# Optimization experiments

Measured on AMD Instinct MI355X. Metric: run time of the kernel, lower is better.

The kernel has to match this reference:

```python
import jax, jax.numpy as jnp
import numpy as np

D_MODEL = 768
N_HEADS = 12
D_K = D_MODEL // N_HEADS
NEG_INF = -1e9


def setup_inputs() -> dict:
    key = jax.random.key(0)
    ks = jax.random.split(key, 7)
    B, S = 4, 2048
    x = jax.random.normal(ks[0], (B, S, D_MODEL), dtype=jnp.float32)
    # causal mask, broadcastable to [B, H, S, S]
    mask = jnp.tril(jnp.ones((S, S), dtype=bool))[None, None, :, :]
    scale = 1.0 / np.sqrt(D_MODEL)
    Wq = jax.random.normal(ks[1], (D_MODEL, D_MODEL), dtype=jnp.float32) * scale
    bq = jnp.zeros((D_MODEL,), dtype=jnp.float32)
    Wk = jax.random.normal(ks[2], (D_MODEL, D_MODEL), dtype=jnp.float32) * scale
    bk = jnp.zeros((D_MODEL,), dtype=jnp.float32)
    Wv = jax.random.normal(ks[3], (D_MODEL, D_MODEL), dtype=jnp.float32) * scale
    bv = jnp.zeros((D_MODEL,), dtype=jnp.float32)
    return {"x": x, "mask": mask, "Wq": Wq, "bq": bq, "Wk": Wk, "bk": bk, "Wv": Wv, "bv": bv}


def reference(x, mask, Wq, bq, Wk, bk, Wv, bv):
    B, S, _ = x.shape
    # projections (torch Linear: y = x @ W.T + b)
    q = (x @ Wq.T + bq).reshape(B, S, N_HEADS, D_K)
    k = (x @ Wk.T + bk).reshape(B, S, N_HEADS, D_K)
    v = (x @ Wv.T + bv).reshape(B, S, N_HEADS, D_K)
    # scores: [B, H, S, S]
    scores = jnp.einsum("bqhd,bkhd->bhqk", q, k) / jnp.sqrt(jnp.float32(D_K))
    scores = jnp.where(mask, scores, NEG_INF)
    probs = jax.nn.softmax(scores, axis=-1)
    # attention: [B, H, S, D_K] -> [B, S, d_model]
    attn = jnp.einsum("bhqk,bkhd->bqhd", probs, v).reshape(B, S, D_MODEL)
    return attn
```

## Files before the change

### kernel.cpp

```cpp
#include <hip/hip_runtime.h>
#include <math.h>


#define S_LEN 2048
#define BATCH 4
#define HEADS 12
#define DM 768
#define DK 64
#define BH (BATCH*HEADS)
#define MROWS (BATCH*S_LEN)
#define QSCALE 0.1803368801111244f

typedef __attribute__((ext_vector_type(8))) short short8;
typedef __attribute__((ext_vector_type(4))) float floatx4;
typedef __attribute__((ext_vector_type(16))) float floatx16;
typedef __attribute__((ext_vector_type(4))) unsigned int uintx4;
typedef __attribute__((address_space(3))) unsigned char lds_byte;
typedef __attribute__((address_space(1))) const unsigned char glob_byte;

__device__ __forceinline__ unsigned short f2bf(float f) {
  union { float f; unsigned int u; } a; a.f = f;
  unsigned int u = a.u;
  return (unsigned short)((u + 0x7fffu + ((u >> 16) & 1u)) >> 16);
}

__global__ __launch_bounds__(256) void cast_all(
    const float* __restrict__ x,
    const float* __restrict__ w0, const float* __restrict__ w1,
    const float* __restrict__ w2,
    unsigned short* __restrict__ xb, unsigned short* __restrict__ wb) {
  const int NX = MROWS * DM, NW = DM * DM;
  int i = (blockIdx.x * 256 + threadIdx.x) * 4;
  const float* src; unsigned short* dst; int off;
  if (i < NX) { src = x; dst = xb; off = i; }
  else {
    int kk = i - NX; int s = kk / NW; off = kk - s * NW;
    src = (s == 0) ? w0 : (s == 1) ? w1 : w2;
    dst = wb + (size_t)s * NW;
  }
  float4 v = *(const float4*)(src + off);
  ushort4 o;
  o.x = f2bf(v.x); o.y = f2bf(v.y); o.z = f2bf(v.z); o.w = f2bf(v.w);
  *(ushort4*)(dst + off) = o;
}

__global__ __launch_bounds__(256) void qkv_gemm(
    const unsigned short* __restrict__ xb,
    const unsigned short* __restrict__ wb,
    const float* __restrict__ bq, const float* __restrict__ bk,
    const float* __restrict__ bv,
    unsigned short* __restrict__ qo,
    unsigned short* __restrict__ ko,
    unsigned short* __restrict__ vto) {
  __shared__ unsigned short a_lds[2 * 128 * 32];
  __shared__ unsigned short b_lds[2 * 128 * 32];
  const int mat = blockIdx.z;
  const int tid = threadIdx.x;
  const int wave = tid >> 6, lane = tid & 63, quad = lane >> 4, ln = lane & 15;
  const int wm = wave & 1, wn = wave >> 1;
  const int m_blk = blockIdx.x * 128, n_blk = blockIdx.y * 128;
  const unsigned short* w = wb + (size_t)mat * DM * DM;
  const int srow_i[2] = { (0 * 256 + wave * 64 + lane) >> 2,
                          (1 * 256 + wave * 64 + lane) >> 2 };
  const int sq = (lane & 3) * 8;

  const floatx4 fz = {0.f, 0.f, 0.f, 0.f};
  floatx4 acc[4][4];
#pragma unroll
  for (int mg = 0; mg < 4; mg++)
#pragma unroll
    for (int c = 0; c < 4; c++) acc[mg][c] = fz;

  for (int k0 = 0; k0 < DM; k0 += 64) {
#pragma unroll
    for (int p = 0; p < 2; p++)
#pragma unroll
      for (int i = 0; i < 2; i++) {
        const int cbase = i * 256 + wave * 64;
        const int row = srow_i[i];
        __builtin_amdgcn_global_load_lds(
            (glob_byte*)(xb + (size_t)(m_blk + row) * DM + k0 + p * 32 + sq),
            (lds_byte*)(a_lds + p * 4096 + cbase * 8), 16, 0, 0);
        __builtin_amdgcn_global_load_lds(
            (glob_byte*)(w + (size_t)(n_blk + row) * DM + k0 + p * 32 + sq),
            (lds_byte*)(b_lds + p * 4096 + cbase * 8), 16, 0, 0);
      }
    __syncthreads();

    short8 af[4][2], bf[4][2];
#pragma unroll
    for (int mg = 0; mg < 4; mg++)
#pragma unroll
      for (int p = 0; p < 2; p++)
        af[mg][p] = *(const short8*)(a_lds + p * 4096 + (wm * 64 + mg * 16 + ln) * 32 + quad * 8);
#pragma unroll
    for (int c = 0; c < 4; c++)
#pragma unroll
      for (int p = 0; p < 2; p++)
        bf[c][p] = *(const short8*)(b_lds + p * 4096 + (wn * 64 + c * 16 + ln) * 32 + quad * 8);
#pragma unroll
    for (int mg = 0; mg < 4; mg++)
#pragma unroll
      for (int c = 0; c < 4; c++) {
        acc[mg][c] = __builtin_amdgcn_mfma_f32_16x16x32_bf16(af[mg][0], bf[c][0], acc[mg][c], 0, 0, 0);
        acc[mg][c] = __builtin_amdgcn_mfma_f32_16x16x32_bf16(af[mg][1], bf[c][1], acc[mg][c], 0, 0, 0);
      }
    __syncthreads();
  }

  const float* bias = (mat == 0) ? bq : (mat == 1) ? bk : bv;
  const float oscale = (mat == 0) ? QSCALE : 1.0f;
  const int m_base = m_blk + wm * 64, n_base = n_blk + wn * 64;
#pragma unroll
  for (int mg = 0; mg < 4; mg++)
#pragma unroll
    for (int c = 0; c < 4; c++) {
      int gn = n_base + c * 16 + ln;
      int hd = gn >> 6, d = gn & 63;
      float bias_v = bias[gn] * oscale;
      int gm0 = m_base + mg * 16 + quad * 4;
      int bb = gm0 >> 11, s0 = gm0 & (S_LEN - 1);
      if (mat == 2) {
        ushort4 pk;
        pk.x = f2bf(acc[mg][c][0] + bias_v);
        pk.y = f2bf(acc[mg][c][1] + bias_v);
        pk.z = f2bf(acc[mg][c][2] + bias_v);
        pk.w = f2bf(acc[mg][c][3] + bias_v);
        *(ushort4*)(vto + (((size_t)(bb * HEADS + hd)) * DK + d) * S_LEN + s0) = pk;
      } else {
        unsigned short* dst = (mat == 0 ? qo : ko) +
            (((size_t)(bb * HEADS + hd)) * S_LEN + s0) * DK + d;
#pragma unroll
        for (int r = 0; r < 4; r++)
          dst[(size_t)r * DK] = f2bf(acc[mg][c][r] * oscale + bias_v);
      }
    }
}

__global__ __launch_bounds__(256) void flash_attn(
    const unsigned short* __restrict__ q,
    const unsigned short* __restrict__ k,
    const unsigned short* __restrict__ vt,
    float* __restrict__ out) {
  __shared__ unsigned short k_lds[2][64 * 64];
  __shared__ unsigned short v_lds[2][64 * 64];
  const int id0 = blockIdx.x;
  const int rr = id0 >> 8, jj = id0 & 255;
  const int g = (rr == 0) ? jj : (rr == 1) ? (511 - jj) : (512 + jj);
  const int bh = g % BH;
  const int qt = (S_LEN / 128 - 1) - (g / BH);
  const int q0 = qt * 128;
  const int tid = threadIdx.x;
  const int wave = tid >> 6, lane = tid & 63;
  const int l31 = lane & 31, hi = lane >> 5;
  const unsigned short* qp = q + (size_t)bh * S_LEN * DK;
  const unsigned char* kpb = (const unsigned char*)(k  + (size_t)bh * S_LEN * DK);
  const unsigned char* vpb = (const unsigned char*)(vt + (size_t)bh * DK * S_LEN);
  const int qr_base = q0 + wave * 32;

  const floatx16 fz16 = {0.f,0.f,0.f,0.f,0.f,0.f,0.f,0.f,
                         0.f,0.f,0.f,0.f,0.f,0.f,0.f,0.f};

  short8 ones;
#pragma unroll
  for (int j = 0; j < 8; j++) ones[j] = (short)0x3F80;

  short8 aq[4];
#pragma unroll
  for (int ks = 0; ks < 4; ks++)
    aq[ks] = *(const short8*)(qp + (size_t)(qr_base + l31) * DK + ks * 16 + hi * 8);

  floatx16 o0 = fz16, o1 = fz16, lacc = fz16;

  const int sc0 = tid, sc1 = 256 + tid;
  const int sr[2]  = { sc0 >> 3, sc1 >> 3 };
  const int ssb[2] = { ((sc0 & 7) * 16) ^ ((sr[0] & 7) << 4),
                       ((sc1 & 7) * 16) ^ ((sr[1] & 7) << 4) };

  auto stage = [&](int nb, int k0) {
    unsigned short* kd = &k_lds[nb][0];
    unsigned short* vd = &v_lds[nb][0];
#pragma unroll
    for (int i = 0; i < 2; i++) {
      const int cbase = i * 256 + wave * 64;
      __builtin_amdgcn_global_load_lds(
          (glob_byte*)(kpb + (size_t)(k0 + sr[i]) * 128 + ssb[i]),
          (lds_byte*)(kd + cbase * 8), 16, 0, 0);
      __builtin_amdgcn_global_load_lds(
          (glob_byte*)(vpb + (size_t)sr[i] * (S_LEN * 2) + k0 * 2 + ssb[i]),
          (lds_byte*)(vd + cbase * 8), 16, 0, 0);
    }
  };

  const int xr = (l31 & 7) << 4;

  auto body = [&](int k0, auto nbc) {
    constexpr int nb = decltype(nbc)::value;
    const unsigned char* kb = (const unsigned char*)&k_lds[nb][0];
    const unsigned char* vb = (const unsigned char*)&v_lds[nb][0];
    const bool domask = (k0 + 63 > qr_base);
#pragma unroll
    for (int kg = 0; kg < 2; kg++) {
      floatx16 sc = fz16;
      __builtin_amdgcn_s_setprio(1);
#pragma unroll
      for (int ks = 0; ks < 4; ks++) {
        short8 kf = *(const short8*)(kb + (kg * 32 + l31) * 128 + ((ks * 32 + hi * 16) ^ xr));
        sc = __builtin_amdgcn_mfma_f32_32x32x16_bf16(kf, aq[ks], sc, 0, 0, 0);
      }
      __builtin_amdgcn_s_setprio(0);
      float pv[16];
      const int qr = qr_base + l31;
#pragma unroll
      for (int r = 0; r < 16; r++) {
        float e2 = exp2f(sc[r]);
        if (domask) {
          int key = k0 + kg * 32 + (r & 3) + 8 * (r >> 2) + 4 * hi;
          e2 = (key <= qr) ? e2 : 0.f;
        }
        pv[r] = e2;
      }
      unsigned int dw[4][2];
#pragma unroll
      for (int b = 0; b < 4; b++)
#pragma unroll
        for (int c = 0; c < 2; c++)
          asm("v_cvt_pk_bf16_f32 %0, %1, %2"
              : "=v"(dw[b][c]) : "v"(pv[4 * b + 2 * c]), "v"(pv[4 * b + 2 * c + 1]));
#pragma unroll
      for (int ks2 = 0; ks2 < 2; ks2++) {
        unsigned int a0 = dw[2 * ks2][0], a1 = dw[2 * ks2][1];
        unsigned int b0 = dw[2 * ks2 + 1][0], b1 = dw[2 * ks2 + 1][1];
        asm("v_permlane32_swap_b32 %0, %1" : "+v"(a0), "+v"(b0));
        asm("v_permlane32_swap_b32 %0, %1" : "+v"(a1), "+v"(b1));
        union { uintx4 u; short8 s; } ap;
        ap.u = (uintx4){a0, a1, b0, b1};
        short8 vf0 = *(const short8*)(vb + (0 * 32 + l31) * 128 + ((kg * 64 + ks2 * 32 + hi * 16) ^ xr));
        short8 vf1 = *(const short8*)(vb + (1 * 32 + l31) * 128 + ((kg * 64 + ks2 * 32 + hi * 16) ^ xr));
        __builtin_amdgcn_s_setprio(1);
        o0 = __builtin_amdgcn_mfma_f32_32x32x16_bf16(ap.s, vf0, o0, 0, 0, 0);
        o1 = __builtin_amdgcn_mfma_f32_32x32x16_bf16(ap.s, vf1, o1, 0, 0, 0);
        lacc = __builtin_amdgcn_mfma_f32_32x32x16_bf16(ap.s, ones, lacc, 0, 0, 0);
        __builtin_amdgcn_s_setprio(0);
      }
    }
  };

  const auto B0 = std::integral_constant<int, 0>{};
  const auto B1 = std::integral_constant<int, 1>{};
  const int nt = (q0 + 128) / 64;
  const int qmax = qr_base + 31;
  stage(0, 0);
  __syncthreads();
  int t = 0;
#pragma unroll 1
  for (; t + 2 < nt; t += 2) {
    stage(1, (t + 1) * 64);
    if (t * 64 <= qmax) body(t * 64, B0);
    __syncthreads();
    stage(0, (t + 2) * 64);
    if ((t + 1) * 64 <= qmax) body((t + 1) * 64, B1);
    __syncthreads();
  }
  stage(1, (t + 1) * 64);
  if (t * 64 <= qmax) body(t * 64, B0);
  __syncthreads();
  if ((t + 1) * 64 <= qmax) body((t + 1) * 64, B1);

  const int b = bh / HEADS, hd = bh % HEADS;
#pragma unroll
  for (int r = 0; r < 16; r++) {
    float inv = 1.f / lacc[r];
    int qrow = qr_base + (r & 3) + 8 * (r >> 2) + 4 * hi;
    float* orow = out + ((size_t)(b * S_LEN + qrow)) * DM + hd * DK;
    orow[l31]      = o0[r] * inv;
    orow[32 + l31] = o1[r] * inv;
  }
}

extern "C" void kernel_launch(void* const* d_in, const int* in_sizes, int n_in,
                              void* d_out, int out_size, void* d_ws, size_t ws_size,
                              hipStream_t stream) {
  const float* x  = (const float*)d_in[0];
  const float* Wq = (const float*)d_in[2];
  const float* bq = (const float*)d_in[3];
  const float* Wk = (const float*)d_in[4];
  const float* bk = (const float*)d_in[5];
  const float* Wv = (const float*)d_in[6];
  const float* bv = (const float*)d_in[7];
  float* out = (float*)d_out;

  const int NX = MROWS * DM;
  const int NW = DM * DM;
  const size_t NQK = (size_t)BH * S_LEN * DK;
  unsigned short* xb = (unsigned short*)d_ws;
  unsigned short* wb = xb + NX;
  unsigned short* qo = wb + 3 * NW;
  unsigned short* ko = qo + NQK;
  unsigned short* vt = ko + NQK;

  cast_all<<<(NX + 3 * NW) / 4 / 256, 256, 0, stream>>>(x, Wq, Wk, Wv, xb, wb);

  qkv_gemm<<<dim3(MROWS / 128, DM / 128, 3), 256, 0, stream>>>(
      xb, wb, bq, bk, bv, qo, ko, vt);

  flash_attn<<<dim3((S_LEN / 128) * BH), 256, 0, stream>>>(qo, ko, vt, out);
}
```

Measured before the change: 209.1 us.

## Triple-buffer K/V tiles in flash attention with partial vmcnt waits

Moves the K/V LDS staging from double to triple buffering. Loads run two tiles ahead, and each iteration waits only for the older tile with s_waitcnt vmcnt(4) before a raw barrier, so global-to-LDS loads overlap more of the compute. The cost is 50% more LDS per block, which may lower occupancy. Buffers are now rotated through runtime pointers instead of compile-time indices, which can add address arithmetic.

```diff
diff --git a/kernel.cpp b/kernel.cpp
--- a/kernel.cpp
+++ b/kernel.cpp
@@ -142,8 +142,8 @@
     const unsigned short* __restrict__ k,
     const unsigned short* __restrict__ vt,
     float* __restrict__ out) {
-  __shared__ unsigned short k_lds[2][64 * 64];
-  __shared__ unsigned short v_lds[2][64 * 64];
+  __shared__ unsigned short k_lds[3][64 * 64];
+  __shared__ unsigned short v_lds[3][64 * 64];
   const int id0 = blockIdx.x;
   const int rr = id0 >> 8, jj = id0 & 255;
   const int g = (rr == 0) ? jj : (rr == 1) ? (511 - jj) : (512 + jj);
@@ -177,9 +177,7 @@
   const int ssb[2] = { ((sc0 & 7) * 16) ^ ((sr[0] & 7) << 4),
                        ((sc1 & 7) * 16) ^ ((sr[1] & 7) << 4) };
 
-  auto stage = [&](int nb, int k0) {
-    unsigned short* kd = &k_lds[nb][0];
-    unsigned short* vd = &v_lds[nb][0];
+  auto stage = [&](unsigned short* kd, unsigned short* vd, int k0) {
 #pragma unroll
     for (int i = 0; i < 2; i++) {
       const int cbase = i * 256 + wave * 64;
@@ -194,10 +192,9 @@
 
   const int xr = (l31 & 7) << 4;
 
-  auto body = [&](int k0, auto nbc) {
-    constexpr int nb = decltype(nbc)::value;
-    const unsigned char* kb = (const unsigned char*)&k_lds[nb][0];
-    const unsigned char* vb = (const unsigned char*)&v_lds[nb][0];
+  auto body = [&](int k0, const unsigned short* kbp, const unsigned short* vbp) {
+    const unsigned char* kb = (const unsigned char*)kbp;
+    const unsigned char* vb = (const unsigned char*)vbp;
     const bool domask = (k0 + 63 > qr_base);
 #pragma unroll
     for (int kg = 0; kg < 2; kg++) {
@@ -246,26 +243,32 @@
     }
   };
 
-  const auto B0 = std::integral_constant<int, 0>{};
-  const auto B1 = std::integral_constant<int, 1>{};
   const int nt = (q0 + 128) / 64;
   const int qmax = qr_base + 31;
-  stage(0, 0);
+
+  unsigned short *kA = &k_lds[0][0], *kB = &k_lds[1][0], *kC = &k_lds[2][0];
+  unsigned short *vA = &v_lds[0][0], *vB = &v_lds[1][0], *vC = &v_lds[2][0];
+
+  stage(kA, vA, 0);
+  stage(kB, vB, 64);
   __syncthreads();
-  int t = 0;
+
 #pragma unroll 1
-  for (; t + 2 < nt; t += 2) {
-    stage(1, (t + 1) * 64);
-    if (t * 64 <= qmax) body(t * 64, B0);
-    __syncthreads();
-    stage(0, (t + 2) * 64);
-    if ((t + 1) * 64 <= qmax) body((t + 1) * 64, B1);
-    __syncthreads();
+  for (int t = 0; t < nt; ++t) {
+    if (t + 2 < nt) stage(kC, vC, (t + 2) * 64);
+    if (t * 64 <= qmax) body(t * 64, kA, vA);
+    if (t + 1 < nt) {
+      if (t + 2 < nt) {
+        asm volatile("s_waitcnt vmcnt(4)" ::: "memory");
+      } else {
+        asm volatile("s_waitcnt vmcnt(0)" ::: "memory");
+      }
+      __builtin_amdgcn_s_barrier();
+      __builtin_amdgcn_sched_barrier(0);
+    }
+    unsigned short* tk = kA; kA = kB; kB = kC; kC = tk;
+    unsigned short* tv = vA; vA = vB; vB = vC; vC = tv;
   }
-  stage(1, (t + 1) * 64);
-  if (t * 64 <= qmax) body(t * 64, B0);
-  __syncthreads();
-  if ((t + 1) * 64 <= qmax) body((t + 1) * 64, B1);
 
   const int b = bh / HEADS, hd = bh % HEADS;
 #pragma unroll
```

Result: no change. 209.2 us (+0.0%).

## Double-buffer QKV GEMM LDS tiles to overlap global loads with MFMA

Applied to the files above, without the earlier changes.

Restructures the QKV projection GEMM main loop so each 32-wide K slice is loaded into one LDS buffer while MFMAs run on the other, with a prologue and epilogue around the loop. The goal is to hide global-to-LDS load latency behind compute instead of stalling on a barrier before each 64-wide step. The cost is more barriers, each covering half as much compute per iteration, and the correctness of the buffer handoff rests on the barrier placement.

```diff
diff --git a/kernel.cpp b/kernel.cpp
--- a/kernel.cpp
+++ b/kernel.cpp
@@ -52,8 +52,8 @@
     unsigned short* __restrict__ qo,
     unsigned short* __restrict__ ko,
     unsigned short* __restrict__ vto) {
-  __shared__ unsigned short a_lds[2 * 128 * 32];
-  __shared__ unsigned short b_lds[2 * 128 * 32];
+  __shared__ unsigned short a_lds[2][128 * 32];
+  __shared__ unsigned short b_lds[2][128 * 32];
   const int mat = blockIdx.z;
   const int tid = threadIdx.x;
   const int wave = tid >> 6, lane = tid & 63, quad = lane >> 4, ln = lane & 15;
@@ -71,42 +71,56 @@
 #pragma unroll
     for (int c = 0; c < 4; c++) acc[mg][c] = fz;
 
-  for (int k0 = 0; k0 < DM; k0 += 64) {
-#pragma unroll
-    for (int p = 0; p < 2; p++)
-#pragma unroll
-      for (int i = 0; i < 2; i++) {
-        const int cbase = i * 256 + wave * 64;
-        const int row = srow_i[i];
-        __builtin_amdgcn_global_load_lds(
-            (glob_byte*)(xb + (size_t)(m_blk + row) * DM + k0 + p * 32 + sq),
-            (lds_byte*)(a_lds + p * 4096 + cbase * 8), 16, 0, 0);
-        __builtin_amdgcn_global_load_lds(
-            (glob_byte*)(w + (size_t)(n_blk + row) * DM + k0 + p * 32 + sq),
-            (lds_byte*)(b_lds + p * 4096 + cbase * 8), 16, 0, 0);
-      }
+  auto stage = [&](auto nbc, int k0) {
+    constexpr int nb = decltype(nbc)::value;
+#pragma unroll
+    for (int i = 0; i < 2; i++) {
+      const int cbase = i * 256 + wave * 64;
+      const int row = srow_i[i];
+      __builtin_amdgcn_global_load_lds(
+          (glob_byte*)(xb + (size_t)(m_blk + row) * DM + k0 + sq),
+          (lds_byte*)(&a_lds[nb][0] + cbase * 8), 16, 0, 0);
+      __builtin_amdgcn_global_load_lds(
+          (glob_byte*)(w + (size_t)(n_blk + row) * DM + k0 + sq),
+          (lds_byte*)(&b_lds[nb][0] + cbase * 8), 16, 0, 0);
+    }
+  };
+
+  auto compute = [&](auto nbc) {
+    constexpr int nb = decltype(nbc)::value;
+    short8 af[4], bf[4];
+#pragma unroll
+    for (int mg = 0; mg < 4; mg++)
+      af[mg] = *(const short8*)(&a_lds[nb][0] + (wm * 64 + mg * 16 + ln) * 32 + quad * 8);
+#pragma unroll
+    for (int c = 0; c < 4; c++)
+      bf[c] = *(const short8*)(&b_lds[nb][0] + (wn * 64 + c * 16 + ln) * 32 + quad * 8);
+#pragma unroll
+    for (int mg = 0; mg < 4; mg++)
+#pragma unroll
+      for (int c = 0; c < 4; c++)
+        acc[mg][c] = __builtin_amdgcn_mfma_f32_16x16x32_bf16(af[mg], bf[c], acc[mg][c], 0, 0, 0);
+  };
+
+  const auto B0 = std::integral_constant<int, 0>{};
+  const auto B1 = std::integral_constant<int, 1>{};
+
+  stage(B0, 0);
+  __syncthreads();
+  int k0 = 0;
+#pragma unroll 1
+  for (; k0 + 64 < DM; k0 += 64) {
+    stage(B1, k0 + 32);
+    compute(B0);
     __syncthreads();
-
-    short8 af[4][2], bf[4][2];
-#pragma unroll
-    for (int mg = 0; mg < 4; mg++)
-#pragma unroll
-      for (int p = 0; p < 2; p++)
-        af[mg][p] = *(const short8*)(a_lds + p * 4096 + (wm * 64 + mg * 16 + ln) * 32 + quad * 8);
-#pragma unroll
-    for (int c = 0; c < 4; c++)
-#pragma unroll
-      for (int p = 0; p < 2; p++)
-        bf[c][p] = *(const short8*)(b_lds + p * 4096 + (wn * 64 + c * 16 + ln) * 32 + quad * 8);
-#pragma unroll
-    for (int mg = 0; mg < 4; mg++)
-#pragma unroll
-      for (int c = 0; c < 4; c++) {
-        acc[mg][c] = __builtin_amdgcn_mfma_f32_16x16x32_bf16(af[mg][0], bf[c][0], acc[mg][c], 0, 0, 0);
-        acc[mg][c] = __builtin_amdgcn_mfma_f32_16x16x32_bf16(af[mg][1], bf[c][1], acc[mg][c], 0, 0, 0);
-      }
+    stage(B0, k0 + 64);
+    compute(B1);
     __syncthreads();
   }
+  stage(B1, k0 + 32);
+  compute(B0);
+  __syncthreads();
+  compute(B1);
 
   const float* bias = (mat == 0) ? bq : (mat == 1) ? bk : bv;
   const float oscale = (mat == 0) ? QSCALE : 1.0f;
```

After: 212.7 us. No clear change (+1.7%).
